# Performance work log

Measured on AMD Instinct MI355X. Metric: run time of the kernel, lower is better.

## Reference

```python
import jax, jax.numpy as jnp
import numpy as np

# ---- static config (matches init_kwargs) ----
BATCH = 8; SEQ_LEN = 1024; ENC_IN = 7; PRED_LEN = 96
D_MODEL = 512; N_HEADS = 8; D_HEAD = D_MODEL // N_HEADS
D_FF = 2048; E_LAYERS = 2; FACTOR = 5
PATCH = 16; STRIDE = 8; PAD = 8
N_PATCH = (SEQ_LEN + PAD - PATCH) // STRIDE + 1  # 128
NF = D_MODEL * N_PATCH


def _sin_pe(n, d):
    # sinusoidal positional embedding (Informer/TSLib PositionalEmbedding)
    pos = np.arange(n, dtype=np.float32)[:, None]
    div = np.exp(np.arange(0, d, 2, dtype=np.float32) * (-np.log(10000.0) / d))
    pe = np.zeros((n, d), dtype=np.float32)
    pe[:, 0::2] = np.sin(pos * div)
    pe[:, 1::2] = np.cos(pos * div)
    return jnp.asarray(pe)


def _ln(x, g, b, eps=1e-5):
    m = x.mean(-1, keepdims=True)
    v = x.var(-1, keepdims=True)
    return (x - m) / jnp.sqrt(v + eps) * g + b


def _prob_attention(q, k, v, layer_idx):
    # Informer ProbAttention, mask_flag=False. q,k,v: [B,H,L,Dh]
    B, H, L, Dh = q.shape
    u = min(int(FACTOR * np.ceil(np.log(L))), L)  # sample_k == n_top here (L_Q == L_K)
    skey = jax.random.fold_in(jax.random.key(42), layer_idx)
    samp = jax.random.randint(skey, (L, u), 0, L)          # random keys per query
    k_s = k[:, :, samp, :]                                  # [B,H,L,u,Dh]
    qk_s = jnp.einsum('bhld,bhlsd->bhls', q, k_s)           # sampled scores
    M = qk_s.max(-1) - qk_s.mean(-1)                        # sparsity measure [B,H,L]
    top = jax.lax.top_k(M, u)[1]                            # active query idx [B,H,u]
    q_r = jnp.take_along_axis(q, top[..., None], axis=2)    # [B,H,u,Dh]
    scores = jnp.einsum('bhud,bhld->bhul', q_r, k) / jnp.sqrt(jnp.asarray(Dh, q.dtype))
    attn = jax.nn.softmax(scores, axis=-1)
    upd = jnp.einsum('bhul,bhld->bhud', attn, v)            # [B,H,u,Dh]
    ctx = jnp.broadcast_to(v.mean(axis=2, keepdims=True), (B, H, L, Dh))
    bi = jnp.arange(B)[:, None, None]
    hi = jnp.arange(H)[None, :, None]
    ctx = ctx.at[bi, hi, top].set(upd)                      # scatter updated queries
    return ctx


def reference(x_enc, x_mark_enc, x_dec, x_mark_dec, patch_W,
              Wq, bq, Wk, bk, Wv, bv, Wo, bo,
              c1W, c1b, c2W, c2b, ln1g, ln1b, ln2g, ln2b,
              encg, encb, headW, headb):
    B, L, C = x_enc.shape
    # Normalize('Stat'): per-series mean/std over time
    mean = x_enc.mean(axis=1, keepdims=True)
    std = jnp.sqrt(x_enc.var(axis=1, keepdims=True) + 1e-5)
    xn = (x_enc - mean) / std
    # PatchEmbedding: [B,C,L] -> replication-pad -> unfold -> linear + pos emb
    xc = jnp.pad(xn.transpose(0, 2, 1), ((0, 0), (0, 0), (0, PAD)), mode='edge')
    idx = np.arange(N_PATCH)[:, None] * STRIDE + np.arange(PATCH)
    tok = xc[:, :, idx].reshape(B * C, N_PATCH, PATCH) @ patch_W.T  # [BC,N,dm]
    tok = tok + _sin_pe(N_PATCH, D_MODEL)
    # Transformer encoder with ProbAttention
    for l in range(E_LAYERS):
        Beff, N, _ = tok.shape
        q = (tok @ Wq[l].T + bq[l]).reshape(Beff, N, N_HEADS, D_HEAD).transpose(0, 2, 1, 3)
        k = (tok @ Wk[l].T + bk[l]).reshape(Beff, N, N_HEADS, D_HEAD).transpose(0, 2, 1, 3)
        v = (tok @ Wv[l].T + bv[l]).reshape(Beff, N, N_HEADS, D_HEAD).transpose(0, 2, 1, 3)
        ctx = _prob_attention(q, k, v, l).transpose(0, 2, 1, 3).reshape(Beff, N, D_MODEL)
        x1 = _ln(tok + ctx @ Wo[l].T + bo[l], ln1g[l], ln1b[l])
        y = jax.nn.gelu(x1 @ c1W[l].T + c1b[l], approximate=False)  # conv1d k=1 == linear
        y = y @ c2W[l].T + c2b[l]
        tok = _ln(x1 + y, ln2g[l], ln2b[l])
    tok = _ln(tok, encg, encb)
    # FlattenHead: [B,C,N,dm] -> [B,C,dm,N] -> flatten -> linear -> [B,pred,C]
    feat = tok.reshape(B, C, N_PATCH, D_MODEL).transpose(0, 1, 3, 2).reshape(B, C, NF)
    dec = (feat @ headW.T + headb).transpose(0, 2, 1)
    return dec * std + mean  # de-normalize


def setup_inputs():
    key = jax.random.key(0)
    ks = iter(jax.random.split(key, 40))
    def rn(shape, s=0.02):
        return jax.random.normal(next(ks), shape, jnp.float32) * s
    return {
        'x_enc': jax.random.normal(next(ks), (BATCH, SEQ_LEN, ENC_IN), jnp.float32),
        'x_mark_enc': jax.random.normal(next(ks), (BATCH, SEQ_LEN, 4), jnp.float32),
        'x_dec': jax.random.normal(next(ks), (BATCH, 144, ENC_IN), jnp.float32),
        'x_mark_dec': jax.random.normal(next(ks), (BATCH, 144, 4), jnp.float32),
        'patch_W': rn((D_MODEL, PATCH)),
        'Wq': rn((E_LAYERS, D_MODEL, D_MODEL)), 'bq': jnp.zeros((E_LAYERS, D_MODEL)),
        'Wk': rn((E_LAYERS, D_MODEL, D_MODEL)), 'bk': jnp.zeros((E_LAYERS, D_MODEL)),
        'Wv': rn((E_LAYERS, D_MODEL, D_MODEL)), 'bv': jnp.zeros((E_LAYERS, D_MODEL)),
        'Wo': rn((E_LAYERS, D_MODEL, D_MODEL)), 'bo': jnp.zeros((E_LAYERS, D_MODEL)),
        'c1W': rn((E_LAYERS, D_FF, D_MODEL)), 'c1b': jnp.zeros((E_LAYERS, D_FF)),
        'c2W': rn((E_LAYERS, D_MODEL, D_FF)), 'c2b': jnp.zeros((E_LAYERS, D_MODEL)),
        'ln1g': jnp.ones((E_LAYERS, D_MODEL)), 'ln1b': jnp.zeros((E_LAYERS, D_MODEL)),
        'ln2g': jnp.ones((E_LAYERS, D_MODEL)), 'ln2b': jnp.zeros((E_LAYERS, D_MODEL)),
        'encg': jnp.ones((D_MODEL,)), 'encb': jnp.zeros((D_MODEL,)),
        'headW': rn((PRED_LEN, NF)), 'headb': jnp.zeros((PRED_LEN,)),
    }
```

## Files before the change

kernel.cpp:

```cpp
#include <hip/hip_runtime.h>
#include <math.h>
#include <stdint.h>

#define SEQ   1024
#define CIN   7
#define NB    8
#define BC    56
#define NP    128
#define DM    512
#define NH    8
#define DH    64
#define DFF   2048
#define U     25
#define NTOK  (BC*NP)
#define PE_COEF (-9.210340371976184f / 512.0f)
#define HKB   256
#define HNB   256

typedef __attribute__((ext_vector_type(8))) short short8;
typedef __attribute__((ext_vector_type(4))) float f32x4;

__device__ __forceinline__ short f2bf(float x) {
    union { float f; uint32_t u; } v; v.f = x;
    uint32_t r = v.u + 0x7FFFu + ((v.u >> 16) & 1u);
    return (short)(r >> 16);
}
__device__ __forceinline__ float bf2f(short x) {
    union { uint32_t u; float f; } v; v.u = ((uint32_t)(uint16_t)x) << 16;
    return v.f;
}

__device__ __forceinline__ void gl_lds16(const void* g, void* s) {
    __builtin_amdgcn_global_load_lds((const __attribute__((address_space(1))) void*)g,
                                     (__attribute__((address_space(3))) void*)s, 16, 0, 0);
}

__global__ void stats_kernel(const float* __restrict__ x, float* __restrict__ mean,
                             float* __restrict__ stdv) {
    int bc = blockIdx.x; int b = bc / CIN, c = bc % CIN;
    const float* base = x + (size_t)b * SEQ * CIN + c;
    float s = 0.f, ss = 0.f;
    for (int i = threadIdx.x; i < SEQ; i += 256) {
        float v = base[(size_t)i * CIN];
        s += v; ss += v * v;
    }
    __shared__ float rs[256], rss[256];
    rs[threadIdx.x] = s; rss[threadIdx.x] = ss; __syncthreads();
    for (int o = 128; o > 0; o >>= 1) {
        if (threadIdx.x < o) { rs[threadIdx.x] += rs[threadIdx.x + o]; rss[threadIdx.x] += rss[threadIdx.x + o]; }
        __syncthreads();
    }
    if (threadIdx.x == 0) {
        float m = rs[0] / SEQ;
        float v = rss[0] / SEQ - m * m;
        mean[bc] = m;
        stdv[bc] = sqrtf(v + 1e-5f);
    }
}

__device__ __forceinline__ void tf_round(uint32_t& x0, uint32_t& x1, uint32_t r) {
    x0 += x1; x1 = (x1 << r) | (x1 >> (32u - r)); x1 ^= x0;
}
__device__ void threefry2x32(uint32_t k0, uint32_t k1, uint32_t x0, uint32_t x1,
                             uint32_t& o0, uint32_t& o1) {
    uint32_t ks[3] = { k0, k1, k0 ^ k1 ^ 0x1BD11BDAu };
    x0 += ks[0]; x1 += ks[1];
    const uint32_t rotA[4] = {13u, 15u, 26u, 6u}, rotB[4] = {17u, 29u, 16u, 24u};
    #pragma unroll
    for (int i = 0; i < 5; i++) {
        const uint32_t* rr = (i & 1) ? rotB : rotA;
        tf_round(x0, x1, rr[0]); tf_round(x0, x1, rr[1]);
        tf_round(x0, x1, rr[2]); tf_round(x0, x1, rr[3]);
        x0 += ks[(i + 1) % 3];
        x1 += ks[(i + 2) % 3] + (uint32_t)(i + 1);
    }
    o0 = x0; o1 = x1;
}

__global__ void prep_weights(const float* __restrict__ Wq, const float* __restrict__ Wk,
                             const float* __restrict__ Wv, const float* __restrict__ bq,
                             const float* __restrict__ bk, const float* __restrict__ bv,
                             const float* __restrict__ Wo, const float* __restrict__ c1W,
                             const float* __restrict__ c2W,
                             short* __restrict__ wqkv, float* __restrict__ bqkv,
                             short* __restrict__ wo_b, short* __restrict__ c1w_b,
                             short* __restrict__ c2w_b, int* __restrict__ samp) {
    int blk = blockIdx.x, tid = threadIdx.x;
    if (blk < 1536) {
        int idx = blk * 256 + tid;
        int k4 = idx & 127;
        int n  = (idx >> 7) % 1536;
        int l  = idx / (1536 * 128);
        int sel3 = n >> 9;
        int nn = n & 511;
        const float* src = sel3 == 0 ? Wq : sel3 == 1 ? Wk : Wv;
        float4 v = *(const float4*)(src + ((size_t)l * DM + nn) * DM + k4 * 4);
        short4 o; o.x = f2bf(v.x); o.y = f2bf(v.y); o.z = f2bf(v.z); o.w = f2bf(v.w);
        *(short4*)(wqkv + ((size_t)l * 1536 + n) * DM + k4 * 4) = o;
        if (k4 == 0) {
            const float* bsrc = sel3 == 0 ? bq : sel3 == 1 ? bk : bv;
            bqkv[l * 1536 + n] = bsrc[l * DM + nn];
        }
    } else if (blk < 6144) {
        const float* in; short* out; int i;
        if (blk < 2048)      { in = Wo;  out = wo_b;  i = (blk - 1536) * 256 + tid; }
        else if (blk < 4096) { in = c1W; out = c1w_b; i = (blk - 2048) * 256 + tid; }
        else                 { in = c2W; out = c2w_b; i = (blk - 4096) * 256 + tid; }
        float4 v = ((const float4*)in)[i];
        short4 o; o.x = f2bf(v.x); o.y = f2bf(v.y); o.z = f2bf(v.z); o.w = f2bf(v.w);
        ((short4*)out)[i] = o;
    } else {
        int l = blk - 6144;
        uint32_t s0, s1; threefry2x32(0u, 42u, 0u, (uint32_t)l, s0, s1);
        uint32_t a0, a1, b0, b1;
        threefry2x32(s0, s1, 0u, 2u, a0, a1);
        threefry2x32(s0, s1, 1u, 3u, b0, b1);
        uint32_t k20 = a1, k21 = b1;
        for (int i = tid; i < 1600; i += 256) {
            uint32_t o0, o1;
            threefry2x32(k20, k21, (uint32_t)i, (uint32_t)(1600 + i), o0, o1);
            samp[l * 3200 + i]        = (int)(o0 & 127u);
            samp[l * 3200 + 1600 + i] = (int)(o1 & 127u);
        }
    }
}

__global__ void patch_embed(const float* __restrict__ x, const float* __restrict__ pw,
                            const float* __restrict__ mean, const float* __restrict__ stdv,
                            float* __restrict__ tok, short* __restrict__ tokb) {
    int p = blockIdx.x, bc = blockIdx.y;
    int b = bc / CIN, c = bc % CIN;
    __shared__ float xs[16];
    if (threadIdx.x < 16) {
        int i = p * 8 + threadIdx.x;
        if (i > SEQ - 1) i = SEQ - 1;
        xs[threadIdx.x] = (x[(size_t)b * SEQ * CIN + (size_t)i * CIN + c] - mean[bc]) / stdv[bc];
    }
    __syncthreads();
    for (int d = threadIdx.x; d < DM; d += blockDim.x) {
        float acc = 0.f;
        const float* wr = pw + d * 16;
        #pragma unroll
        for (int t = 0; t < 16; t++) acc += xs[t] * wr[t];
        int k2 = d & ~1;
        float ang = (float)p * __expf((float)k2 * PE_COEF);
        acc += (d & 1) ? __cosf(ang) : __sinf(ang);
        size_t idx = ((size_t)bc * NP + p) * DM + d;
        tok[idx] = acc;
        tokb[idx] = f2bf(acc);
    }
}

template<int ACT, int OBF>
__global__ __launch_bounds__(256) void gemm_mfma(const short* __restrict__ A,
                                                 const short* __restrict__ W,
                                                 const float* __restrict__ bias,
                                                 float* __restrict__ Cf,
                                                 short* __restrict__ Cb,
                                                 int M, int N, int K) {
    __shared__ short LDSU[2][16384];
    int tid = threadIdx.x;
    int w = tid >> 6, lane = tid & 63;
    int row0 = blockIdx.x * 128, col0 = blockIdx.y * 128;
    int wrow = (w >> 1) * 64, wcol = (w & 1) * 64;
    int nt = K >> 6;
    f32x4 acc[4][4] = {};

    auto stage = [&](int b, int kt) {
        #pragma unroll
        for (int i = 0; i < 4; i++) {
            int L = i * 4096 + w * 1024 + lane * 16;
            int row = L >> 7;
            int cb  = L & 127;
            int scb = cb ^ ((row & 7) << 4);
            gl_lds16(A + (size_t)(row0 + row) * K + kt + (scb >> 1),
                     (char*)&LDSU[b][0] + i * 4096 + w * 1024);
            gl_lds16(W + (size_t)(col0 + row) * K + kt + (scb >> 1),
                     (char*)&LDSU[b][8192] + i * 4096 + w * 1024);
        }
    };

    stage(0, 0);
    __syncthreads();
    int cur = 0;
    for (int t = 0; t < nt; t++) {
        if (t + 1 < nt) stage(cur ^ 1, (t + 1) * 64);
        const char* Ab = (const char*)&LDSU[cur][0];
        const char* Bb = (const char*)&LDSU[cur][8192];
        #pragma unroll
        for (int ks = 0; ks < 2; ks++) {
            int cb = ks * 64 + ((lane >> 4) << 4);
            short8 af[4], bfr[4];
            #pragma unroll
            for (int m = 0; m < 4; m++) {
                int r = wrow + m * 16 + (lane & 15);
                af[m] = *(const short8*)(Ab + r * 128 + (cb ^ ((r & 7) << 4)));
            }
            #pragma unroll
            for (int n = 0; n < 4; n++) {
                int r = wcol + n * 16 + (lane & 15);
                bfr[n] = *(const short8*)(Bb + r * 128 + (cb ^ ((r & 7) << 4)));
            }
            #pragma unroll
            for (int m = 0; m < 4; m++)
                #pragma unroll
                for (int n = 0; n < 4; n++)
                    acc[m][n] = __builtin_amdgcn_mfma_f32_16x16x32_bf16(af[m], bfr[n], acc[m][n], 0, 0, 0);
        }
        __syncthreads();
        cur ^= 1;
    }

    #pragma unroll
    for (int m = 0; m < 4; m++) {
        int rbase = row0 + wrow + m * 16 + ((lane >> 4) << 2);
        #pragma unroll
        for (int n = 0; n < 4; n++) {
            int col = col0 + wcol + n * 16 + (lane & 15);
            float bval = bias[col];
            #pragma unroll
            for (int j = 0; j < 4; j++) {
                float v = acc[m][n][j] + bval;
                if (ACT == 1) {
                    float u = 0.7978845608f * (v + 0.044715f * v * v * v);
                    float e = exp2f(2.8853900817779268f * u);
                    v = v - v / (e + 1.0f);
                }
                if (OBF) Cb[(size_t)(rbase + j) * N + col] = f2bf(v);
                else     Cf[(size_t)(rbase + j) * N + col] = v;
            }
        }
    }
}

__global__ __launch_bounds__(256) void gemm_mfma64(const short* __restrict__ A,
                                                   const short* __restrict__ W,
                                                   const float* __restrict__ bias,
                                                   float* __restrict__ Cf,
                                                   int M, int N, int K) {
    __shared__ short LDSU[2][12288];
    int tid = threadIdx.x;
    int w = tid >> 6, lane = tid & 63;
    int row0 = blockIdx.x * 64, col0 = blockIdx.y * 128;
    int nt = K >> 6;
    f32x4 acc[4][2] = {};

    auto stage = [&](int b, int kt) {
        #pragma unroll
        for (int i = 0; i < 2; i++) {
            int L = (i * 4 + w) * 1024 + lane * 16;
            int row = L >> 7, cb = L & 127;
            int scb = cb ^ ((row & 7) << 4);
            gl_lds16(A + (size_t)(row0 + row) * K + kt + (scb >> 1),
                     (char*)&LDSU[b][0] + (i * 4 + w) * 1024);
        }
        #pragma unroll
        for (int i = 0; i < 4; i++) {
            int L = (i * 4 + w) * 1024 + lane * 16;
            int row = L >> 7, cb = L & 127;
            int scb = cb ^ ((row & 7) << 4);
            gl_lds16(W + (size_t)(col0 + row) * K + kt + (scb >> 1),
                     (char*)&LDSU[b][4096] + (i * 4 + w) * 1024);
        }
    };

    stage(0, 0);
    __syncthreads();
    int cur = 0;
    for (int t = 0; t < nt; t++) {
        if (t + 1 < nt) stage(cur ^ 1, (t + 1) * 64);
        const char* Ab = (const char*)&LDSU[cur][0];
        const char* Bb = (const char*)&LDSU[cur][4096];
        #pragma unroll
        for (int ks = 0; ks < 2; ks++) {
            int cb = ks * 64 + ((lane >> 4) << 4);
            short8 af[4], bfr[2];
            #pragma unroll
            for (int m = 0; m < 4; m++) {
                int r = m * 16 + (lane & 15);
                af[m] = *(const short8*)(Ab + r * 128 + (cb ^ ((r & 7) << 4)));
            }
            #pragma unroll
            for (int n = 0; n < 2; n++) {
                int r = w * 32 + n * 16 + (lane & 15);
                bfr[n] = *(const short8*)(Bb + r * 128 + (cb ^ ((r & 7) << 4)));
            }
            #pragma unroll
            for (int m = 0; m < 4; m++)
                #pragma unroll
                for (int n = 0; n < 2; n++)
                    acc[m][n] = __builtin_amdgcn_mfma_f32_16x16x32_bf16(af[m], bfr[n], acc[m][n], 0, 0, 0);
        }
        __syncthreads();
        cur ^= 1;
    }

    #pragma unroll
    for (int m = 0; m < 4; m++) {
        int rbase = row0 + m * 16 + ((lane >> 4) << 2);
        #pragma unroll
        for (int n = 0; n < 2; n++) {
            int col = col0 + w * 32 + n * 16 + (lane & 15);
            float bval = bias[col];
            #pragma unroll
            for (int j = 0; j < 4; j++)
                Cf[(size_t)(rbase + j) * N + col] = acc[m][n][j] + bval;
        }
    }
}

__global__ __launch_bounds__(256, 2) void attn_fused(const short* __restrict__ qkvb,
                                                     const int* __restrict__ samp,
                                                     short* __restrict__ ctxb) {
    __shared__ float Sbuf[64 * 130];
    __shared__ short Vt[64 * 128];
    __shared__ short Kls[128 * 64];
    __shared__ float Mv[128];
    __shared__ int   topl[32];
    __shared__ float vmean[64];
    __shared__ float vpart[256];

    float* Stop = Sbuf;
    short* Pb   = (short*)(Sbuf + 32 * 130);

    int bh = blockIdx.x, bc = bh >> 3, h = bh & 7;
    int tid = threadIdx.x, w = tid >> 6, lane = tid & 63;
    const short* base = qkvb + (size_t)bc * NP * 1536 + h * DH;
    short* cbase = ctxb + (size_t)bc * NP * DM + h * DH;

    for (int e = tid; e < 1024; e += 256) {
        int row = e >> 3, c8 = e & 7;
        short8 kv = *(const short8*)(base + (size_t)row * 1536 + 512 + c8 * 8);
        *(short8*)((char*)Kls + row * 128 + ((c8 * 16) ^ ((row & 7) << 4))) = kv;
        short8 vv = *(const short8*)(base + (size_t)row * 1536 + 1024 + c8 * 8);
        #pragma unroll
        for (int j = 0; j < 8; j++) {
            int d = c8 * 8 + j;
            *(short*)((char*)Vt + d * 256 + ((2 * row) ^ ((d & 7) << 4))) = vv[j];
        }
    }
    __syncthreads();
    {
        int d = tid & 63, part = tid >> 6;
        float s = 0.f;
        #pragma unroll
        for (int i4 = 0; i4 < 4; i4++) {
            short8 v = *(const short8*)((char*)Vt + d * 256 + ((part * 64 + i4 * 16) ^ ((d & 7) << 4)));
            #pragma unroll
            for (int j = 0; j < 8; j++) s += bf2f(v[j]);
        }
        vpart[part * 64 + d] = s;
    }

    for (int half = 0; half < 2; half++) {
        int ar = half * 64 + 16 * w + (lane & 15);
        const short* qp = base + (size_t)ar * 1536;
        short8 a0 = *(const short8*)(qp + (lane >> 4) * 8);
        short8 a1 = *(const short8*)(qp + 32 + (lane >> 4) * 8);
        #pragma unroll 2
        for (int ct = 0; ct < 8; ct++) {
            int br = ct * 16 + (lane & 15);
            int cb0 = (lane >> 4) * 16;
            short8 b0 = *(const short8*)((char*)Kls + br * 128 + (cb0 ^ ((br & 7) << 4)));
            short8 b1 = *(const short8*)((char*)Kls + br * 128 + ((cb0 + 64) ^ ((br & 7) << 4)));
            f32x4 acc = {};
            acc = __builtin_amdgcn_mfma_f32_16x16x32_bf16(a0, b0, acc, 0, 0, 0);
            acc = __builtin_amdgcn_mfma_f32_16x16x32_bf16(a1, b1, acc, 0, 0, 0);
            int r0 = 16 * w + ((lane >> 4) << 2);
            int c = ct * 16 + (lane & 15);
            #pragma unroll
            for (int j = 0; j < 4; j++) Sbuf[(r0 + j) * 130 + c] = acc[j] * 0.125f;
        }
        __syncthreads();
        if (tid < 64) {
            int r = half * 64 + tid;
            const int* sp = samp + r * U;
            const float* Srow = &Sbuf[tid * 130];
            float mx = -1e30f, sm = 0.f;
            #pragma unroll
            for (int s = 0; s < U; s++) { float v = Srow[sp[s]]; mx = fmaxf(mx, v); sm += v; }
            Mv[r] = mx - sm * (1.0f / U);
        } else if (half == 0 && tid < 128) {
            int d = tid - 64;
            vmean[d] = (vpart[d] + vpart[64 + d] + vpart[128 + d] + vpart[192 + d]) * (1.0f / 128.0f);
        }
        __syncthreads();
    }

    if (w == 0) {
        float v0 = Mv[lane], v1 = Mv[lane + 64];
        for (int it = 0; it < U; it++) {
            float bv; int bi;
            if (v1 > v0) { bv = v1; bi = lane + 64; } else { bv = v0; bi = lane; }
            #pragma unroll
            for (int o = 32; o > 0; o >>= 1) {
                float ov = __shfl_xor(bv, o);
                int   oi = __shfl_xor(bi, o);
                if (ov > bv || (ov == bv && oi < bi)) { bv = ov; bi = oi; }
            }
            if (lane == 0) topl[it] = bi;
            if (bi == lane) v0 = -1e30f;
            if (bi == lane + 64) v1 = -1e30f;
        }
    } else {
        for (int e = tid - 64; e < 128 * 16; e += 192) {
            int n = e >> 4, c4 = e & 15;
            short4 o;
            o.x = f2bf(vmean[c4 * 4 + 0]); o.y = f2bf(vmean[c4 * 4 + 1]);
            o.z = f2bf(vmean[c4 * 4 + 2]); o.w = f2bf(vmean[c4 * 4 + 3]);
            *(short4*)(cbase + (size_t)n * DM + c4 * 4) = o;
        }
    }
    __syncthreads();

    {
        int rt = w & 1, cth = w >> 1;
        int u = rt * 16 + (lane & 15);
        int qrow = topl[u < U ? u : U - 1];
        const short* qp = base + (size_t)qrow * 1536;
        short8 a0 = *(const short8*)(qp + (lane >> 4) * 8);
        short8 a1 = *(const short8*)(qp + 32 + (lane >> 4) * 8);
        #pragma unroll
        for (int cti = 0; cti < 4; cti++) {
            int ct = cth * 4 + cti;
            int br = ct * 16 + (lane & 15);
            int cb0 = (lane >> 4) * 16;
            short8 b0 = *(const short8*)((char*)Kls + br * 128 + (cb0 ^ ((br & 7) << 4)));
            short8 b1 = *(const short8*)((char*)Kls + br * 128 + ((cb0 + 64) ^ ((br & 7) << 4)));
            f32x4 acc = {};
            acc = __builtin_amdgcn_mfma_f32_16x16x32_bf16(a0, b0, acc, 0, 0, 0);
            acc = __builtin_amdgcn_mfma_f32_16x16x32_bf16(a1, b1, acc, 0, 0, 0);
            int r0 = rt * 16 + ((lane >> 4) << 2);
            int c = ct * 16 + (lane & 15);
            #pragma unroll
            for (int j = 0; j < 4; j++) Stop[(r0 + j) * 130 + c] = acc[j] * 0.125f;
        }
    }
    __syncthreads();

    for (int e = tid; e < 7 * 128; e += 256)
        Pb[(25 + (e >> 7)) * 128 + (e & 127)] = 0;
    for (int it = w; it < U; it += 4) {
        float s0 = Stop[it * 130 + lane], s1 = Stop[it * 130 + 64 + lane];
        float mx = fmaxf(s0, s1);
        #pragma unroll
        for (int o = 32; o > 0; o >>= 1) mx = fmaxf(mx, __shfl_xor(mx, o));
        float e0 = expf(s0 - mx), e1 = expf(s1 - mx);
        float sum = e0 + e1;
        #pragma unroll
        for (int o = 32; o > 0; o >>= 1) sum += __shfl_xor(sum, o);
        float inv = 1.0f / sum;
        int sw = (it & 7) << 4;
        *(short*)((char*)Pb + it * 256 + ((2 * lane) ^ sw))        = f2bf(e0 * inv);
        *(short*)((char*)Pb + it * 256 + ((2 * (64 + lane)) ^ sw)) = f2bf(e1 * inv);
    }
    __syncthreads();

    #pragma unroll
    for (int t = w * 2; t < w * 2 + 2; t++) {
        int rt = t >> 2, ct = t & 3;
        int pr = rt * 16 + (lane & 15);
        int vr = ct * 16 + (lane & 15);
        f32x4 acc = {};
        #pragma unroll
        for (int ks = 0; ks < 4; ks++) {
            int off = ks * 64 + (lane >> 4) * 16;
            short8 a = *(const short8*)((char*)Pb + pr * 256 + (off ^ ((pr & 7) << 4)));
            short8 b = *(const short8*)((char*)Vt + vr * 256 + (off ^ ((vr & 7) << 4)));
            acc = __builtin_amdgcn_mfma_f32_16x16x32_bf16(a, b, acc, 0, 0, 0);
        }
        int u0 = rt * 16 + ((lane >> 4) << 2), d = ct * 16 + (lane & 15);
        #pragma unroll
        for (int j = 0; j < 4; j++) {
            int u = u0 + j;
            if (u < U) cbase[(size_t)topl[u] * DM + d] = f2bf(acc[j]);
        }
    }
}

__global__ __launch_bounds__(256) void residual_ln(const float* __restrict__ a,
                                                   const float* __restrict__ b,
                                                   const float* __restrict__ b2,
                                                   const float* __restrict__ g,
                                                   const float* __restrict__ beta,
                                                   float* __restrict__ out,
                                                   short* __restrict__ outb) {
    int row = blockIdx.x;
    int tid = threadIdx.x;
    const float* ar = a + (size_t)row * DM;
    float x0 = ar[tid], x1 = ar[tid + 256];
    if (b) {
        const float* br = b + (size_t)row * DM;
        x0 += br[tid]; x1 += br[tid + 256];
    }
    if (b2) {
        const float* br = b2 + (size_t)row * DM;
        x0 += br[tid]; x1 += br[tid + 256];
    }
    __shared__ float rs[256], rss[256];
    rs[tid] = x0 + x1; rss[tid] = x0 * x0 + x1 * x1; __syncthreads();
    for (int o = 128; o > 0; o >>= 1) {
        if (tid < o) { rs[tid] += rs[tid + o]; rss[tid] += rss[tid + o]; }
        __syncthreads();
    }
    float m = rs[0] / DM;
    float var = rss[0] / DM - m * m;
    float r = rsqrtf(var + 1e-5f);
    float y0 = (x0 - m) * r * g[tid] + beta[tid];
    float y1 = (x1 - m) * r * g[tid + 256] + beta[tid + 256];
    out[(size_t)row * DM + tid]       = y0;
    out[(size_t)row * DM + tid + 256] = y1;
    if (outb) {
        outb[(size_t)row * DM + tid]       = f2bf(y0);
        outb[(size_t)row * DM + tid + 256] = f2bf(y1);
    }
}

__global__ void transpose_tok(const float* __restrict__ tok, short* __restrict__ featb) {
    __shared__ float t[32][33];
    int bc = blockIdx.z, dt = blockIdx.y, pt = blockIdx.x;
    int tx = threadIdx.x, ty = threadIdx.y;
    #pragma unroll
    for (int i = 0; i < 4; i++) {
        int p = pt * 32 + ty + i * 8;
        int d = dt * 32 + tx;
        t[ty + i * 8][tx] = tok[((size_t)bc * NP + p) * DM + d];
    }
    __syncthreads();
    #pragma unroll
    for (int i = 0; i < 4; i++) {
        int d = dt * 32 + ty + i * 8;
        int p = pt * 32 + tx;
        featb[(size_t)bc * (DM * NP) + (size_t)d * NP + p] = f2bf(t[tx][ty + i * 8]);
    }
}

__global__ __launch_bounds__(256) void head_mfma(const float* __restrict__ hw,
                                                 const short* __restrict__ featb,
                                                 float* __restrict__ partial) {
    __shared__ short Als[96 * 64];
    __shared__ short Bls[64 * 64];
    int tid = threadIdx.x;
    int w = tid >> 6, lane = tid & 63;
    int wm = w >> 1, wn = w & 1;
    int kb = blockIdx.x * HKB;
    f32x4 acc[3][2] = {};
    const char* Ab = (const char*)Als;
    const char* Bb = (const char*)Bls;

    for (int kt = 0; kt < HKB; kt += 64) {
        #pragma unroll
        for (int i = 0; i < 6; i++) {
            int s = tid + i * 256;
            int row = s >> 4, c4 = s & 15;
            float4 v = *(const float4*)(hw + (size_t)row * 65536 + kb + kt + c4 * 4);
            short4 o; o.x = f2bf(v.x); o.y = f2bf(v.y); o.z = f2bf(v.z); o.w = f2bf(v.w);
            int boff = row * 128 + ((c4 * 8) ^ ((row & 7) << 4));
            *(short4*)((char*)Als + boff) = o;
        }
        #pragma unroll
        for (int i = 0; i < 4; i++) {
            int s = tid + i * 256;
            int row = s >> 4, c4 = s & 15;
            short4 o;
            if (row < BC) o = *(const short4*)(featb + (size_t)row * 65536 + kb + kt + c4 * 4);
            else { o.x = 0; o.y = 0; o.z = 0; o.w = 0; }
            int boff = row * 128 + ((c4 * 8) ^ ((row & 7) << 4));
            *(short4*)((char*)Bls + boff) = o;
        }
        __syncthreads();
        #pragma unroll
        for (int ks = 0; ks < 2; ks++) {
            int cb = ks * 64 + ((lane >> 4) << 4);
            short8 af[3], bfr[2];
            #pragma unroll
            for (int m = 0; m < 3; m++) {
                int r = wm * 48 + m * 16 + (lane & 15);
                af[m] = *(const short8*)(Ab + r * 128 + (cb ^ ((r & 7) << 4)));
            }
            #pragma unroll
            for (int n = 0; n < 2; n++) {
                int r = wn * 32 + n * 16 + (lane & 15);
                bfr[n] = *(const short8*)(Bb + r * 128 + (cb ^ ((r & 7) << 4)));
            }
            #pragma unroll
            for (int m = 0; m < 3; m++)
                #pragma unroll
                for (int n = 0; n < 2; n++)
                    acc[m][n] = __builtin_amdgcn_mfma_f32_16x16x32_bf16(af[m], bfr[n], acc[m][n], 0, 0, 0);
        }
        __syncthreads();
    }

    float* pb = partial + (size_t)blockIdx.x * (96 * 64);
    #pragma unroll
    for (int m = 0; m < 3; m++) {
        int rbase = wm * 48 + m * 16 + ((lane >> 4) << 2);
        #pragma unroll
        for (int n = 0; n < 2; n++) {
            int col = wn * 32 + n * 16 + (lane & 15);
            #pragma unroll
            for (int j = 0; j < 4; j++)
                pb[(rbase + j) * 64 + col] = acc[m][n][j];
        }
    }
}

__global__ void finalize_a(const float* __restrict__ partial, float* __restrict__ p2) {
    int i = blockIdx.x * 256 + threadIdx.x;
    int s = blockIdx.y;
    const float* p = partial + (size_t)s * 32 * 6144 + i;
    float sum = 0.f;
    #pragma unroll
    for (int b = 0; b < 32; b++) sum += p[(size_t)b * 6144];
    p2[s * 6144 + i] = sum;
}

__global__ void finalize_b(const float* __restrict__ p2, const float* __restrict__ hb,
                           const float* __restrict__ mean, const float* __restrict__ stdv,
                           float* __restrict__ out) {
    int i = blockIdx.x * 256 + threadIdx.x;
    if (i >= NB * 96 * CIN) return;
    int b = i / (96 * CIN);
    int r = i % (96 * CIN);
    int t = r / CIN, c = r % CIN;
    int bc = b * CIN + c;
    int j = t * 64 + bc;
    float s = 0.f;
    #pragma unroll
    for (int k = 0; k < 8; k++) s += p2[k * 6144 + j];
    out[i] = (s + hb[t]) * stdv[bc] + mean[bc];
}

extern "C" void kernel_launch(void* const* d_in, const int* in_sizes, int n_in,
                              void* d_out, int out_size, void* d_ws, size_t ws_size,
                              hipStream_t stream) {
    (void)in_sizes; (void)n_in; (void)out_size; (void)ws_size;
    const float* x_enc   = (const float*)d_in[0];
    const float* patch_W = (const float*)d_in[4];
    const float* Wq  = (const float*)d_in[5];
    const float* bq  = (const float*)d_in[6];
    const float* Wk  = (const float*)d_in[7];
    const float* bk  = (const float*)d_in[8];
    const float* Wv  = (const float*)d_in[9];
    const float* bv  = (const float*)d_in[10];
    const float* Wo  = (const float*)d_in[11];
    const float* bo  = (const float*)d_in[12];
    const float* c1W = (const float*)d_in[13];
    const float* c1b = (const float*)d_in[14];
    const float* c2W = (const float*)d_in[15];
    const float* c2b = (const float*)d_in[16];
    const float* ln1g = (const float*)d_in[17];
    const float* ln1b = (const float*)d_in[18];
    const float* ln2g = (const float*)d_in[19];
    const float* ln2b = (const float*)d_in[20];
    const float* encg = (const float*)d_in[21];
    const float* encb = (const float*)d_in[22];
    const float* headW = (const float*)d_in[23];
    const float* headb = (const float*)d_in[24];
    float* out = (float*)d_out;

    float* ws = (float*)d_ws;
    float* mean = ws + 0;
    float* stdv = ws + 64;
    float* bqkv = ws + 128;
    int*   samp = (int*)(ws + 6144);
    size_t off = 32768;
    const size_t T = (size_t)NTOK * DM;
    float* tok     = ws + off; off += T;
    float* pA      = ws + off; off += T;
    float* x1      = ws + off; off += T;
    float* partial = ws + off; off += T;
    float* p2      = x1;
    short* sbase = (short*)(ws + off);
    size_t soff = 0;
    short* tok_b  = sbase + soff; soff += T;
    short* ctx_b  = sbase + soff; soff += T;
    short* x1_b   = sbase + soff; soff += T;
    short* qkv_b  = sbase + soff; soff += 3 * T;
    short* ffn_b  = sbase + soff; soff += (size_t)NTOK * DFF;
    short* featb  = ffn_b;
    short* wqkv_b = sbase + soff; soff += 2 * 1536 * DM;
    short* wo_b   = sbase + soff; soff += 2 * DM * DM;
    short* c1w_b  = sbase + soff; soff += 2 * (size_t)DFF * DM;
    short* c2w_b  = sbase + soff; soff += 2 * (size_t)DM * DFF;

    stats_kernel<<<BC, 256, 0, stream>>>(x_enc, mean, stdv);
    prep_weights<<<6146, 256, 0, stream>>>(Wq, Wk, Wv, bq, bk, bv, Wo, c1W, c2W,
                                           wqkv_b, bqkv, wo_b, c1w_b, c2w_b, samp);
    patch_embed<<<dim3(NP, BC), 128, 0, stream>>>(x_enc, patch_W, mean, stdv, tok, tok_b);

    for (int l = 0; l < 2; l++) {
        gemm_mfma<0,1><<<dim3(56, 12), 256, 0, stream>>>(tok_b, wqkv_b + (size_t)l * 1536 * DM, bqkv + l * 1536, nullptr, qkv_b, NTOK, 1536, DM);
        attn_fused<<<448, 256, 0, stream>>>(qkv_b, samp + l * 3200, ctx_b);
        gemm_mfma64<<<dim3(112, 4), 256, 0, stream>>>(ctx_b, wo_b + (size_t)l * DM * DM, bo + l * DM, pA, NTOK, DM, DM);
        residual_ln<<<NTOK, 256, 0, stream>>>(tok, pA, nullptr, ln1g + l * DM, ln1b + l * DM, x1, x1_b);
        gemm_mfma<1,1><<<dim3(56, 16), 256, 0, stream>>>(x1_b, c1w_b + (size_t)l * DFF * DM, c1b + l * DFF, nullptr, ffn_b, NTOK, DFF, DM);
        gemm_mfma64<<<dim3(112, 4), 256, 0, stream>>>(ffn_b, c2w_b + (size_t)l * DM * DFF, c2b + l * DM, pA, NTOK, DM, DFF);
        residual_ln<<<NTOK, 256, 0, stream>>>(x1, pA, nullptr, ln2g + l * DM, ln2b + l * DM, tok, tok_b);
    }

    residual_ln<<<NTOK, 256, 0, stream>>>(tok, nullptr, nullptr, encg, encb, tok, nullptr);
    transpose_tok<<<dim3(4, 16, BC), dim3(32, 8), 0, stream>>>(tok, featb);
    head_mfma<<<HNB, 256, 0, stream>>>(headW, featb, partial);
    finalize_a<<<dim3(24, 8), 256, 0, stream>>>(partial, p2);
    finalize_b<<<21, 256, 0, stream>>>(p2, headb, mean, stdv, out);
}
```

Baseline: 318.0 us.

## Fuse residual add and LayerNorm into full-row output-projection and FFN2 GEMMs

Replaces the 64x128-tiled GEMM plus separate residual_ln kernels with a gemm_ln kernel in which each block computes a 32-row by full-512-column tile. Bias, residual add and LayerNorm (and the final encoder norm on the last layer) are applied in registers, so the fp32 intermediate buffer round trip and five extra launches go away. In exchange, weight fragments are read straight from global memory without LDS staging. The grid also shrinks to 224 blocks, which may leave compute units underused and add memory latency in the GEMM main loop.

```diff
diff --git a/kernel.cpp b/kernel.cpp
--- a/kernel.cpp
+++ b/kernel.cpp
@@ -233,80 +233,149 @@
     }
 }
 
-__global__ __launch_bounds__(256) void gemm_mfma64(const short* __restrict__ A,
-                                                   const short* __restrict__ W,
-                                                   const float* __restrict__ bias,
-                                                   float* __restrict__ Cf,
-                                                   int M, int N, int K) {
-    __shared__ short LDSU[2][12288];
-    int tid = threadIdx.x;
-    int w = tid >> 6, lane = tid & 63;
-    int row0 = blockIdx.x * 64, col0 = blockIdx.y * 128;
+template<int SECOND_LN>
+__global__ __launch_bounds__(256) void gemm_ln(const short* __restrict__ A,
+                                               const short* __restrict__ W,
+                                               const float* __restrict__ bias,
+                                               const float* __restrict__ resid,
+                                               const float* __restrict__ g,
+                                               const float* __restrict__ beta,
+                                               const float* __restrict__ g2,
+                                               const float* __restrict__ beta2,
+                                               float* __restrict__ outF,
+                                               short* __restrict__ outB,
+                                               int K) {
+    __shared__ short Als[2][2048];
+    __shared__ float lsum[4][32];
+    __shared__ float lssq[4][32];
+    int tid = threadIdx.x, w = tid >> 6, lane = tid & 63;
+    int cl = lane & 15, lg = lane >> 4;
+    int row0 = blockIdx.x * 32;
     int nt = K >> 6;
-    f32x4 acc[4][2] = {};
-
-    auto stage = [&](int b, int kt) {
-        #pragma unroll
-        for (int i = 0; i < 2; i++) {
-            int L = (i * 4 + w) * 1024 + lane * 16;
-            int row = L >> 7, cb = L & 127;
-            int scb = cb ^ ((row & 7) << 4);
-            gl_lds16(A + (size_t)(row0 + row) * K + kt + (scb >> 1),
-                     (char*)&LDSU[b][0] + (i * 4 + w) * 1024);
-        }
-        #pragma unroll
-        for (int i = 0; i < 4; i++) {
-            int L = (i * 4 + w) * 1024 + lane * 16;
-            int row = L >> 7, cb = L & 127;
-            int scb = cb ^ ((row & 7) << 4);
-            gl_lds16(W + (size_t)(col0 + row) * K + kt + (scb >> 1),
-                     (char*)&LDSU[b][4096] + (i * 4 + w) * 1024);
-        }
+    f32x4 acc[2][8] = {};
+
+    auto stageA = [&](int b, int kt) {
+        int L = tid * 16;
+        int row = L >> 7, cb = L & 127;
+        int scb = cb ^ ((row & 7) << 4);
+        gl_lds16(A + (size_t)(row0 + row) * K + kt + (scb >> 1),
+                 (char*)&Als[b][0] + w * 1024 + lane * 16);
     };
 
-    stage(0, 0);
+    stageA(0, 0);
     __syncthreads();
     int cur = 0;
     for (int t = 0; t < nt; t++) {
-        if (t + 1 < nt) stage(cur ^ 1, (t + 1) * 64);
-        const char* Ab = (const char*)&LDSU[cur][0];
-        const char* Bb = (const char*)&LDSU[cur][4096];
+        if (t + 1 < nt) stageA(cur ^ 1, (t + 1) * 64);
+        const char* Ab = (const char*)&Als[cur][0];
+        int kt = t * 64;
         #pragma unroll
         for (int ks = 0; ks < 2; ks++) {
-            int cb = ks * 64 + ((lane >> 4) << 4);
-            short8 af[4], bfr[2];
-            #pragma unroll
-            for (int m = 0; m < 4; m++) {
-                int r = m * 16 + (lane & 15);
-                af[m] = *(const short8*)(Ab + r * 128 + (cb ^ ((r & 7) << 4)));
-            }
-            #pragma unroll
-            for (int n = 0; n < 2; n++) {
-                int r = w * 32 + n * 16 + (lane & 15);
-                bfr[n] = *(const short8*)(Bb + r * 128 + (cb ^ ((r & 7) << 4)));
-            }
-            #pragma unroll
-            for (int m = 0; m < 4; m++)
+            int cb = ks * 64 + (lg << 4);
+            short8 af0, af1;
+            {
+                int r = cl;
+                af0 = *(const short8*)(Ab + r * 128 + (cb ^ ((r & 7) << 4)));
+                r = 16 + cl;
+                af1 = *(const short8*)(Ab + r * 128 + (cb ^ ((r & 7) << 4)));
+            }
+            #pragma unroll
+            for (int n = 0; n < 8; n++) {
+                int col = w * 128 + n * 16 + cl;
+                short8 bf = *(const short8*)(W + (size_t)col * K + kt + ks * 32 + lg * 8);
+                acc[0][n] = __builtin_amdgcn_mfma_f32_16x16x32_bf16(af0, bf, acc[0][n], 0, 0, 0);
+                acc[1][n] = __builtin_amdgcn_mfma_f32_16x16x32_bf16(af1, bf, acc[1][n], 0, 0, 0);
+            }
+        }
+        __syncthreads();
+        cur ^= 1;
+    }
+
+    int colb = w * 128 + cl;
+    float gv[8], bev[8];
+    #pragma unroll
+    for (int n = 0; n < 8; n++) {
+        int c = colb + n * 16;
+        float bb = bias[c];
+        gv[n] = g[c]; bev[n] = beta[c];
+        #pragma unroll
+        for (int m = 0; m < 2; m++)
+            #pragma unroll
+            for (int j = 0; j < 4; j++)
+                acc[m][n][j] += bb + resid[(size_t)(row0 + m * 16 + lg * 4 + j) * DM + c];
+    }
+
+    #pragma unroll
+    for (int m = 0; m < 2; m++)
+        #pragma unroll
+        for (int j = 0; j < 4; j++) {
+            float s = 0.f, ss = 0.f;
+            #pragma unroll
+            for (int n = 0; n < 8; n++) { float t = acc[m][n][j]; s += t; ss += t * t; }
+            #pragma unroll
+            for (int mk = 1; mk <= 8; mk <<= 1) { s += __shfl_xor(s, mk); ss += __shfl_xor(ss, mk); }
+            if (cl == 0) { lsum[w][m * 16 + lg * 4 + j] = s; lssq[w][m * 16 + lg * 4 + j] = ss; }
+        }
+    __syncthreads();
+    #pragma unroll
+    for (int m = 0; m < 2; m++)
+        #pragma unroll
+        for (int j = 0; j < 4; j++) {
+            int r = m * 16 + lg * 4 + j;
+            float s  = lsum[0][r] + lsum[1][r] + lsum[2][r] + lsum[3][r];
+            float ss = lssq[0][r] + lssq[1][r] + lssq[2][r] + lssq[3][r];
+            float mu = s * (1.0f / DM);
+            float var = ss * (1.0f / DM) - mu * mu;
+            float rstd = rsqrtf(var + 1e-5f);
+            #pragma unroll
+            for (int n = 0; n < 8; n++)
+                acc[m][n][j] = (acc[m][n][j] - mu) * rstd * gv[n] + bev[n];
+        }
+
+    if (SECOND_LN) {
+        #pragma unroll
+        for (int n = 0; n < 8; n++) { int c = colb + n * 16; gv[n] = g2[c]; bev[n] = beta2[c]; }
+        __syncthreads();
+        #pragma unroll
+        for (int m = 0; m < 2; m++)
+            #pragma unroll
+            for (int j = 0; j < 4; j++) {
+                float s = 0.f, ss = 0.f;
                 #pragma unroll
-                for (int n = 0; n < 2; n++)
-                    acc[m][n] = __builtin_amdgcn_mfma_f32_16x16x32_bf16(af[m], bfr[n], acc[m][n], 0, 0, 0);
-        }
-        __syncthreads();
-        cur ^= 1;
-    }
-
-    #pragma unroll
-    for (int m = 0; m < 4; m++) {
-        int rbase = row0 + m * 16 + ((lane >> 4) << 2);
-        #pragma unroll
-        for (int n = 0; n < 2; n++) {
-            int col = col0 + w * 32 + n * 16 + (lane & 15);
-            float bval = bias[col];
-            #pragma unroll
-            for (int j = 0; j < 4; j++)
-                Cf[(size_t)(rbase + j) * N + col] = acc[m][n][j] + bval;
-        }
-    }
+                for (int n = 0; n < 8; n++) { float t = acc[m][n][j]; s += t; ss += t * t; }
+                #pragma unroll
+                for (int mk = 1; mk <= 8; mk <<= 1) { s += __shfl_xor(s, mk); ss += __shfl_xor(ss, mk); }
+                if (cl == 0) { lsum[w][m * 16 + lg * 4 + j] = s; lssq[w][m * 16 + lg * 4 + j] = ss; }
+            }
+        __syncthreads();
+        #pragma unroll
+        for (int m = 0; m < 2; m++)
+            #pragma unroll
+            for (int j = 0; j < 4; j++) {
+                int r = m * 16 + lg * 4 + j;
+                float s  = lsum[0][r] + lsum[1][r] + lsum[2][r] + lsum[3][r];
+                float ss = lssq[0][r] + lssq[1][r] + lssq[2][r] + lssq[3][r];
+                float mu = s * (1.0f / DM);
+                float var = ss * (1.0f / DM) - mu * mu;
+                float rstd = rsqrtf(var + 1e-5f);
+                #pragma unroll
+                for (int n = 0; n < 8; n++)
+                    acc[m][n][j] = (acc[m][n][j] - mu) * rstd * gv[n] + bev[n];
+            }
+    }
+
+    #pragma unroll
+    for (int m = 0; m < 2; m++)
+        #pragma unroll
+        for (int j = 0; j < 4; j++) {
+            size_t row = row0 + m * 16 + lg * 4 + j;
+            #pragma unroll
+            for (int n = 0; n < 8; n++) {
+                float v = acc[m][n][j];
+                outF[row * DM + colb + n * 16] = v;
+                if (outB) outB[row * DM + colb + n * 16] = f2bf(v);
+            }
+        }
 }
 
 __global__ __launch_bounds__(256, 2) void attn_fused(const short* __restrict__ qkvb,
@@ -475,44 +544,6 @@
             int u = u0 + j;
             if (u < U) cbase[(size_t)topl[u] * DM + d] = f2bf(acc[j]);
         }
-    }
-}
-
-__global__ __launch_bounds__(256) void residual_ln(const float* __restrict__ a,
-                                                   const float* __restrict__ b,
-                                                   const float* __restrict__ b2,
-                                                   const float* __restrict__ g,
-                                                   const float* __restrict__ beta,
-                                                   float* __restrict__ out,
-                                                   short* __restrict__ outb) {
-    int row = blockIdx.x;
-    int tid = threadIdx.x;
-    const float* ar = a + (size_t)row * DM;
-    float x0 = ar[tid], x1 = ar[tid + 256];
-    if (b) {
-        const float* br = b + (size_t)row * DM;
-        x0 += br[tid]; x1 += br[tid + 256];
-    }
-    if (b2) {
-        const float* br = b2 + (size_t)row * DM;
-        x0 += br[tid]; x1 += br[tid + 256];
-    }
-    __shared__ float rs[256], rss[256];
-    rs[tid] = x0 + x1; rss[tid] = x0 * x0 + x1 * x1; __syncthreads();
-    for (int o = 128; o > 0; o >>= 1) {
-        if (tid < o) { rs[tid] += rs[tid + o]; rss[tid] += rss[tid + o]; }
-        __syncthreads();
-    }
-    float m = rs[0] / DM;
-    float var = rss[0] / DM - m * m;
-    float r = rsqrtf(var + 1e-5f);
-    float y0 = (x0 - m) * r * g[tid] + beta[tid];
-    float y1 = (x1 - m) * r * g[tid + 256] + beta[tid + 256];
-    out[(size_t)row * DM + tid]       = y0;
-    out[(size_t)row * DM + tid + 256] = y1;
-    if (outb) {
-        outb[(size_t)row * DM + tid]       = f2bf(y0);
-        outb[(size_t)row * DM + tid + 256] = f2bf(y1);
     }
 }
 
@@ -668,7 +699,6 @@
     size_t off = 32768;
     const size_t T = (size_t)NTOK * DM;
     float* tok     = ws + off; off += T;
-    float* pA      = ws + off; off += T;
     float* x1      = ws + off; off += T;
     float* partial = ws + off; off += T;
     float* p2      = x1;
@@ -693,14 +723,20 @@
     for (int l = 0; l < 2; l++) {
         gemm_mfma<0,1><<<dim3(56, 12), 256, 0, stream>>>(tok_b, wqkv_b + (size_t)l * 1536 * DM, bqkv + l * 1536, nullptr, qkv_b, NTOK, 1536, DM);
         attn_fused<<<448, 256, 0, stream>>>(qkv_b, samp + l * 3200, ctx_b);
-        gemm_mfma64<<<dim3(112, 4), 256, 0, stream>>>(ctx_b, wo_b + (size_t)l * DM * DM, bo + l * DM, pA, NTOK, DM, DM);
-        residual_ln<<<NTOK, 256, 0, stream>>>(tok, pA, nullptr, ln1g + l * DM, ln1b + l * DM, x1, x1_b);
+        gemm_ln<0><<<224, 256, 0, stream>>>(ctx_b, wo_b + (size_t)l * DM * DM, bo + l * DM,
+                                            tok, ln1g + l * DM, ln1b + l * DM,
+                                            nullptr, nullptr, x1, x1_b, DM);
         gemm_mfma<1,1><<<dim3(56, 16), 256, 0, stream>>>(x1_b, c1w_b + (size_t)l * DFF * DM, c1b + l * DFF, nullptr, ffn_b, NTOK, DFF, DM);
-        gemm_mfma64<<<dim3(112, 4), 256, 0, stream>>>(ffn_b, c2w_b + (size_t)l * DM * DFF, c2b + l * DM, pA, NTOK, DM, DFF);
-        residual_ln<<<NTOK, 256, 0, stream>>>(x1, pA, nullptr, ln2g + l * DM, ln2b + l * DM, tok, tok_b);
-    }
-
-    residual_ln<<<NTOK, 256, 0, stream>>>(tok, nullptr, nullptr, encg, encb, tok, nullptr);
+        if (l == 0)
+            gemm_ln<0><<<224, 256, 0, stream>>>(ffn_b, c2w_b + (size_t)l * DM * DFF, c2b + l * DM,
+                                                x1, ln2g + l * DM, ln2b + l * DM,
+                                                nullptr, nullptr, tok, tok_b, DFF);
+        else
+            gemm_ln<1><<<224, 256, 0, stream>>>(ffn_b, c2w_b + (size_t)l * DM * DFF, c2b + l * DM,
+                                                x1, ln2g + l * DM, ln2b + l * DM,
+                                                encg, encb, tok, nullptr, DFF);
+    }
+
     transpose_tok<<<dim3(4, 16, BC), dim3(32, 8), 0, stream>>>(tok, featb);
     head_mfma<<<HNB, 256, 0, stream>>>(headW, featb, partial);
     finalize_a<<<dim3(24, 8), 256, 0, stream>>>(partial, p2);
```

Result: slower. 423.4 us (+33.1%).
